# Kernel tuning notes

Measured on AMD Instinct MI355X. Metric: run time of the kernel, lower is better.

## Reference

```python
import jax, jax.numpy as jnp
import numpy as np

NUM_HEADS = 16
NUM_T = 8
L1D = 16  # img_size // patch_size


def _freqs_1d(dim, end, base=10000.0):
    f = 1.0 / (base ** (jnp.arange(0, dim, 2, dtype=jnp.float32) / dim))  # [dim/2]
    ang = jnp.outer(jnp.arange(end, dtype=jnp.float32), f)                # [end, dim/2]
    return jnp.cos(ang), jnp.sin(ang)


def _freqs_2d(dim, h, w, base=10000.0):
    f = 1.0 / (base ** (jnp.arange(0, dim, 4, dtype=jnp.float32)[: dim // 4] / dim))  # [dim/4]
    ax = jnp.outer(jnp.arange(w, dtype=jnp.float32), f)  # [w, dim/4]
    ay = jnp.outer(jnp.arange(h, dtype=jnp.float32), f)  # [h, dim/4]
    # flatten order: position index = y*w + x
    ang_x = jnp.broadcast_to(ax[None, :, :], (h, w, dim // 4)).reshape(h * w, dim // 4)
    ang_y = jnp.broadcast_to(ay[:, None, :], (h, w, dim // 4)).reshape(h * w, dim // 4)
    ang = jnp.concatenate([ang_x, ang_y], axis=-1)  # [h*w, dim/2]
    return jnp.cos(ang), jnp.sin(ang)


def _rope(x, cos, sin):
    # x: [..., P, d]; cos/sin: [P, d/2]; interleaved complex pairs (x0,x1),(x2,x3),...
    xr, xi = x[..., 0::2], x[..., 1::2]
    or_ = xr * cos - xi * sin
    oi = xr * sin + xi * cos
    return jnp.stack([or_, oi], axis=-1).reshape(x.shape)


def setup_inputs() -> dict:
    key = jax.random.key(0)
    ks = jax.random.split(key, 5)
    H = 1024
    return {
        "x": jax.random.normal(ks[0], (2, 2048, H), dtype=jnp.float32),
        "w_qkv": jax.random.normal(ks[1], (3 * H, H), dtype=jnp.float32) * 0.02,
        "b_qkv": jax.random.normal(ks[2], (3 * H,), dtype=jnp.float32) * 0.02,
        "w_out": jax.random.normal(ks[3], (H, H), dtype=jnp.float32) * 0.02,
        "b_out": jax.random.normal(ks[4], (H,), dtype=jnp.float32) * 0.02,
    }


def reference(x, w_qkv, b_qkv, w_out, b_out):
    B, L, H = x.shape
    n, t = NUM_HEADS, NUM_T
    hd = H // n
    Ls = L // t  # spatial tokens per frame (= L1D*L1D)

    # QKV projection; per-head layout [q|k|v] of size 3*hd (matches torch rearrange+chunk)
    qkv = (x @ w_qkv.T + b_qkv).reshape(B, L, n, 3 * hd)
    q, k, v = qkv[..., :hd], qkv[..., hd:2 * hd], qkv[..., 2 * hd:]

    cos_s, sin_s = _freqs_2d(hd, L1D, L1D)  # [Ls, hd/2]
    cos_t, sin_t = _freqs_1d(hd, t)         # [t, hd/2]

    def to_bntl(a):  # (B, L=t*Ls, n, hd) -> (B, n, t, Ls, hd)
        return a.reshape(B, t, Ls, n, hd).transpose(0, 3, 1, 2, 4)

    q = _rope(to_bntl(q), cos_s, sin_s)
    k = _rope(to_bntl(k), cos_s, sin_s)
    # temporal rope: rotate over t axis
    q = _rope(q.transpose(0, 1, 3, 2, 4), cos_t, sin_t).transpose(0, 1, 3, 2, 4)
    k = _rope(k.transpose(0, 1, 3, 2, 4), cos_t, sin_t).transpose(0, 1, 3, 2, 4)
    q = q.reshape(B, n, L, hd)
    k = k.reshape(B, n, L, hd)
    v = v.transpose(0, 2, 1, 3)  # (B, n, L, hd)

    scores = jnp.einsum('bnqd,bnkd->bnqk', q, k) / jnp.sqrt(jnp.asarray(hd, jnp.float32))
    idx = jnp.arange(L)
    neg = jnp.finfo(jnp.float32).min
    causal = jnp.where(idx[None, :] <= idx[:, None], 0.0, neg)  # [L, L]
    attn = jax.nn.softmax((scores + causal).astype(jnp.float32), axis=-1).astype(x.dtype)

    o = jnp.einsum('bnqk,bnkd->bnqd', attn, v).transpose(0, 2, 1, 3).reshape(B, L, H)
    o = o * jax.nn.sigmoid(o)  # swish
    return o @ w_out.T + b_out
```

## Files before the change

### kernel.cpp

```cpp
#include <hip/hip_runtime.h>
#include <math.h>

#define B_SZ 2
#define L_SEQ 2048
#define H_SZ 1024
#define NH 16
#define HD 64
#define QSCALE 0.18033688011112042f

typedef __attribute__((ext_vector_type(8))) short frag_ab;
typedef __attribute__((ext_vector_type(4))) float frag_cd;
typedef __attribute__((ext_vector_type(8))) unsigned short u16x8;
typedef __attribute__((ext_vector_type(4))) unsigned short u16x4;

__device__ __forceinline__ unsigned short f2bf(float f) {
  unsigned int x = __builtin_bit_cast(unsigned int, f);
  x += 0x7fffu + ((x >> 16) & 1u);
  return (unsigned short)(x >> 16);
}
__device__ __forceinline__ float bf2f(unsigned int u) {
  return __builtin_bit_cast(float, u << 16);
}
__device__ __forceinline__ unsigned int cvt_pk_bf16(float lo, float hi) {
  unsigned int r;
  asm("v_cvt_pk_bf16_f32 %0, %1, %2" : "=v"(r) : "v"(lo), "v"(hi));
  return r;
}
__device__ __forceinline__ void gload16(const void* g, void* l) {
  __builtin_amdgcn_global_load_lds((const __attribute__((address_space(1))) void*)g,
                                   (__attribute__((address_space(3))) void*)l, 16, 0, 0);
}

__device__ __forceinline__ void cvt8(const float* __restrict__ in,
                                     unsigned short* __restrict__ out, int i) {
  float4 a = *(const float4*)&in[i];
  float4 b = *(const float4*)&in[i + 4];
  u16x8 o = {f2bf(a.x), f2bf(a.y), f2bf(a.z), f2bf(a.w),
             f2bf(b.x), f2bf(b.y), f2bf(b.z), f2bf(b.w)};
  *(u16x8*)&out[i] = o;
}

#define SWZ32(row) ((((row) >> 1) & 3) << 3)

__global__ __launch_bounds__(256) void glue_pre_k(
    const float* __restrict__ x, const float* __restrict__ wq, const float* __restrict__ wo,
    unsigned short* __restrict__ xb, unsigned short* __restrict__ wqb,
    unsigned short* __restrict__ wob, float2* __restrict__ ctab) {
  int bx = blockIdx.x, tid = threadIdx.x;
  if (bx < 256) {
    int idx = bx * 256 + tid;
    int j = idx >> 11, l = idx & 2047;
    int ti = l >> 8;
    int s = l & 255;
    float ang_s;
    if (j < 16) ang_s = (float)(s & 15) * powf(10000.f, -(float)j / 16.f);
    else        ang_s = (float)(s >> 4) * powf(10000.f, -(float)(j - 16) / 16.f);
    float ang_t = (float)ti * powf(10000.f, -(float)j / 32.f);
    float a = ang_s + ang_t;
    ctab[idx] = make_float2(cosf(a), sinf(a));
  } else if (bx < 2304) {
    cvt8(x, xb, ((bx - 256) * 256 + tid) * 8);
  } else if (bx < 3840) {
    cvt8(wq, wqb, ((bx - 2304) * 256 + tid) * 8);
  } else {
    cvt8(wo, wob, ((bx - 3840) * 256 + tid) * 8);
  }
}

#define G_ISSUE(k0, bi)                                                        \
  _Pragma("unroll") for (int it = 0; it < 2; ++it) {                           \
    int c = tid + it * 256;                                                    \
    int row = c >> 2, e0 = ((c & 3) * 8) ^ SWZ32(row);                         \
    gload16(A + (size_t)(m0 + row) * K + (k0) + e0, &As[bi][c * 8]);           \
    gload16(W + (size_t)(n0 + row) * K + (k0) + e0, &Ws[bi][c * 8]);           \
  }

__global__ __launch_bounds__(256) void gemm_qkv_fused_k(
    const unsigned short* __restrict__ A, const unsigned short* __restrict__ W,
    const float* __restrict__ bias, const float2* __restrict__ ctab,
    unsigned short* __restrict__ Qb, unsigned short* __restrict__ Kb,
    unsigned short* __restrict__ Vt) {
  const int K = 1024, N = 3072;
  __shared__ unsigned short As[2][128 * 32];
  __shared__ unsigned short Ws[2][128 * 32];
  const frag_cd fzero = {0.f, 0.f, 0.f, 0.f};
  int tid = threadIdx.x;
  int nbx = N >> 7;
  int nwg = gridDim.x;
  int bid = blockIdx.x;
  int qq = nwg >> 3;
  int bidx = (bid & 7) * qq + (bid >> 3);
  int m0 = (bidx / nbx) * 128, n0 = (bidx % nbx) * 128;
  int w = tid >> 6, lane = tid & 63, t = lane & 15, g = lane >> 4;
  int wm = w >> 1, wn = w & 1;
  int fsw = (8 * g) ^ SWZ32(t);
  frag_cd acc[4][4];
#pragma unroll
  for (int mi = 0; mi < 4; ++mi)
#pragma unroll
    for (int ni = 0; ni < 4; ++ni) acc[mi][ni] = fzero;

  G_ISSUE(0, 0);
  __syncthreads();
  int kb = 0;
  for (int k0 = 0; k0 < K; k0 += 32, kb ^= 1) {
    if (k0 + 32 < K) { G_ISSUE(k0 + 32, kb ^ 1); }
    frag_ab af[4], wf[4];
#pragma unroll
    for (int mi = 0; mi < 4; ++mi)
      af[mi] = *(const frag_ab*)&As[kb][(wm * 64 + mi * 16 + t) * 32 + fsw];
#pragma unroll
    for (int ni = 0; ni < 4; ++ni)
      wf[ni] = *(const frag_ab*)&Ws[kb][(wn * 64 + ni * 16 + t) * 32 + fsw];
    __builtin_amdgcn_s_setprio(1);
#pragma unroll
    for (int mi = 0; mi < 4; ++mi)
#pragma unroll
      for (int ni = 0; ni < 4; ++ni)
        acc[mi][ni] = __builtin_amdgcn_mfma_f32_16x16x32_bf16(af[mi], wf[ni], acc[mi][ni], 0, 0, 0);
    __builtin_amdgcn_s_setprio(0);
    __syncthreads();
  }

#pragma unroll
  for (int ni = 0; ni < 4; ++ni) {
    int cb = n0 + wn * 64 + ni * 16;
    int region = (cb >> 6) % 3;
    int head = cb / 192;
    int d = (cb & 63) + t;
    float bv = bias[cb + t];
    if (region == 2) {
#pragma unroll
      for (int mi = 0; mi < 4; ++mi) {
        int row0 = m0 + wm * 64 + mi * 16 + g * 4;
        int bb = row0 >> 11, l0 = row0 & 2047;
        u16x4 ov;
#pragma unroll
        for (int r = 0; r < 4; ++r) ov[r] = f2bf(acc[mi][ni][r] + bv);
        *(u16x4*)&Vt[((size_t)((bb * NH + head) * HD + d)) * L_SEQ + l0] = ov;
      }
    } else {
      float qs = (region == 0) ? QSCALE : 1.f;
      float sgn = (t & 1) ? qs : -qs;
      unsigned short* dst = (region == 0) ? Qb : Kb;
      int j = d >> 1;
#pragma unroll
      for (int mi = 0; mi < 4; ++mi) {
        int row0 = m0 + wm * 64 + mi * 16 + g * 4;
        int bb = row0 >> 11, l0 = row0 & 2047;
        size_t obase = ((size_t)(bb * NH + head) * L_SEQ + l0) * HD + d;
        const float2* cp = ctab + (size_t)j * 2048 + l0;
        float4 v01 = *(const float4*)cp;
        float4 v23 = *(const float4*)(cp + 2);
        float cvec[4] = {v01.x, v01.z, v23.x, v23.z};
        float svec[4] = {v01.y, v01.w, v23.y, v23.w};
#pragma unroll
        for (int r = 0; r < 4; ++r) {
          float v = acc[mi][ni][r] + bv;
          float p = __shfl_xor(v, 1);
          float o = v * (cvec[r] * qs) + p * (svec[r] * sgn);
          dst[obase + (size_t)r * HD] = f2bf(o);
        }
      }
    }
  }
}

__global__ __launch_bounds__(256) void gemm_out_k(
    const unsigned short* __restrict__ A, const unsigned short* __restrict__ W,
    const float* __restrict__ bias, float* __restrict__ C, int M, int N, int K) {
  __shared__ unsigned short As[2][64 * 32];
  __shared__ unsigned short Ws[2][128 * 32];
  const frag_cd fzero = {0.f, 0.f, 0.f, 0.f};
  int tid = threadIdx.x;
  int nbx = N >> 7;
  int nwg = gridDim.x;
  int bid = blockIdx.x;
  int qq = nwg >> 3;
  int bidx = (bid & 7) * qq + (bid >> 3);
  int m0 = (bidx / nbx) * 64, n0 = (bidx % nbx) * 128;
  int w = tid >> 6, lane = tid & 63, t = lane & 15, g = lane >> 4;
  int wm = w >> 1, wn = w & 1;
  int fsw = (8 * g) ^ SWZ32(t);
  frag_cd acc[2][4];
#pragma unroll
  for (int mi = 0; mi < 2; ++mi)
#pragma unroll
    for (int ni = 0; ni < 4; ++ni) acc[mi][ni] = fzero;

#define G_ISSUE2(k0, bi)                                                       \
  {                                                                            \
    int rowA = tid >> 2, e0A = ((tid & 3) * 8) ^ SWZ32(rowA);                  \
    gload16(A + (size_t)(m0 + rowA) * K + (k0) + e0A, &As[bi][tid * 8]);       \
    _Pragma("unroll") for (int it = 0; it < 2; ++it) {                         \
      int c = tid + it * 256;                                                  \
      int row = c >> 2, e0 = ((c & 3) * 8) ^ SWZ32(row);                       \
      gload16(W + (size_t)(n0 + row) * K + (k0) + e0, &Ws[bi][c * 8]);         \
    }                                                                          \
  }

  G_ISSUE2(0, 0);
  __syncthreads();
  int kb = 0;
  for (int k0 = 0; k0 < K; k0 += 32, kb ^= 1) {
    if (k0 + 32 < K) { G_ISSUE2(k0 + 32, kb ^ 1); }
    frag_ab af[2], wf[4];
#pragma unroll
    for (int mi = 0; mi < 2; ++mi)
      af[mi] = *(const frag_ab*)&As[kb][(wm * 32 + mi * 16 + t) * 32 + fsw];
#pragma unroll
    for (int ni = 0; ni < 4; ++ni)
      wf[ni] = *(const frag_ab*)&Ws[kb][(wn * 64 + ni * 16 + t) * 32 + fsw];
    __builtin_amdgcn_s_setprio(1);
#pragma unroll
    for (int mi = 0; mi < 2; ++mi)
#pragma unroll
      for (int ni = 0; ni < 4; ++ni)
        acc[mi][ni] = __builtin_amdgcn_mfma_f32_16x16x32_bf16(af[mi], wf[ni], acc[mi][ni], 0, 0, 0);
    __builtin_amdgcn_s_setprio(0);
    __syncthreads();
  }
#pragma unroll
  for (int mi = 0; mi < 2; ++mi)
#pragma unroll
    for (int ni = 0; ni < 4; ++ni) {
      int col = n0 + wn * 64 + ni * 16 + t;
      float bv = bias[col];
#pragma unroll
      for (int r = 0; r < 4; ++r)
        C[(size_t)(m0 + wm * 32 + mi * 16 + g * 4 + r) * N + col] = acc[mi][ni][r] + bv;
    }
}

__device__ __forceinline__ void attn_tile(
    const unsigned short* __restrict__ Ksb, const unsigned short* __restrict__ Vsb,
    unsigned short* __restrict__ pw,
    const frag_ab* qf, frag_cd* oacc, float& l_run,
    int qrow, bool diag, int kt, int t, int g) {
  const frag_cd cinit = {-32.f, -32.f, -32.f, -32.f};
  frag_cd st[4];
  __builtin_amdgcn_s_setprio(1);
#pragma unroll
  for (int kb = 0; kb < 4; ++kb) {
    frag_ab k0f = *(const frag_ab*)&Ksb[(((kb * 16 + t) * 64) + 8 * g) ^ ((t & 7) << 3)];
    frag_ab k1f = *(const frag_ab*)&Ksb[(((kb * 16 + t) * 64) + 32 + 8 * g) ^ ((t & 7) << 3)];
    st[kb] = __builtin_amdgcn_mfma_f32_16x16x32_bf16(k0f, qf[0], cinit, 0, 0, 0);
    st[kb] = __builtin_amdgcn_mfma_f32_16x16x32_bf16(k1f, qf[1], st[kb], 0, 0, 0);
  }
  __builtin_amdgcn_s_setprio(0);
  float psum = 0.f;
  unsigned int pk[8];
#pragma unroll
  for (int i = 0; i < 8; ++i) {
    int kb = i >> 1, r0 = (2 * i) & 3;
    float x0 = st[kb][r0], x1 = st[kb][r0 + 1];
    if (diag) {
      if ((kt * 64 + kb * 16 + g * 4 + r0) > qrow) x0 = -1e30f;
      if ((kt * 64 + kb * 16 + g * 4 + r0 + 1) > qrow) x1 = -1e30f;
    }
    float p0 = __builtin_amdgcn_exp2f(x0);
    float p1 = __builtin_amdgcn_exp2f(x1);
    psum += p0 + p1;
    pk[i] = cvt_pk_bf16(p0, p1);
  }
  psum += __shfl_xor(psum, 16);
  psum += __shfl_xor(psum, 32);
  l_run += psum;

#pragma unroll
  for (int kb = 0; kb < 4; ++kb) {
    uint2 pr = {pk[kb * 2], pk[kb * 2 + 1]};
    *(uint2*)&pw[(t * 64 + kb * 16 + g * 4) ^ ((t & 7) << 3)] = pr;
  }
  frag_ab pf0 = *(const frag_ab*)&pw[(t * 64 + 8 * g) ^ ((t & 7) << 3)];
  frag_ab pf1 = *(const frag_ab*)&pw[(t * 64 + 32 + 8 * g) ^ ((t & 7) << 3)];
  __builtin_amdgcn_s_setprio(1);
#pragma unroll
  for (int db = 0; db < 4; ++db) {
    frag_ab v0f = *(const frag_ab*)&Vsb[(((db * 16 + t) * 64) + 8 * g) ^ ((t & 7) << 3)];
    frag_ab v1f = *(const frag_ab*)&Vsb[(((db * 16 + t) * 64) + 32 + 8 * g) ^ ((t & 7) << 3)];
    oacc[db] = __builtin_amdgcn_mfma_f32_16x16x32_bf16(v0f, pf0, oacc[db], 0, 0, 0);
    oacc[db] = __builtin_amdgcn_mfma_f32_16x16x32_bf16(v1f, pf1, oacc[db], 0, 0, 0);
  }
  __builtin_amdgcn_s_setprio(0);
}

__global__ __launch_bounds__(512) void attn_mfma_k(
    const unsigned short* __restrict__ Qg, const unsigned short* __restrict__ Kg,
    const unsigned short* __restrict__ Vt, unsigned short* __restrict__ Og) {
  __shared__ unsigned short Ks[2][64 * 64];
  __shared__ unsigned short Vs[2][64 * 64];
  __shared__ unsigned short Ps[8][16 * 64];
  const frag_cd fzero = {0.f, 0.f, 0.f, 0.f};
  int bx = blockIdx.x;
  int qtA = bx & 15;
  int n = (bx >> 4) & 15;
  int b = bx >> 8;
  int qtB = 31 - qtA;
  int tid = threadIdx.x;
  int w = tid >> 6, lane = tid & 63, t = lane & 15, g = lane >> 4;
  int side = w >> 2;
  int qt = side ? qtA : qtB;
  size_t kvbase = ((size_t)(b * NH + n)) * L_SEQ * HD;
  int qrow = qt * 64 + (w & 3) * 16 + t;

  const unsigned short* qp = Qg + kvbase + (size_t)qrow * HD;
  frag_ab qf[2] = {*(const frag_ab*)(qp + 8 * g), *(const frag_ab*)(qp + 32 + 8 * g)};

  frag_cd oacc[4];
#pragma unroll
  for (int db = 0; db < 4; ++db) oacc[db] = fzero;
  float l_run = 0.f;

  int srow = tid >> 3, se0 = (tid & 7) * 8;
  int sdst = (srow * 64 + se0) ^ ((srow & 7) << 3);
  u16x8 kreg = *(const u16x8*)(Kg + kvbase + (size_t)srow * HD + se0);
  u16x8 vreg = *(const u16x8*)(Vt + kvbase + (size_t)srow * L_SEQ + se0);
  *(u16x8*)&Ks[0][sdst] = kreg;
  *(u16x8*)&Vs[0][sdst] = vreg;

  for (int kt = 0; kt <= qtB; ++kt) {
    int cur = kt & 1;
    __syncthreads();
    if (kt < qtB) {
      kreg = *(const u16x8*)(Kg + kvbase + (size_t)((kt + 1) * 64 + srow) * HD + se0);
      vreg = *(const u16x8*)(Vt + kvbase + (size_t)srow * L_SEQ + (kt + 1) * 64 + se0);
    }
    if (kt <= qt)
      attn_tile(&Ks[cur][0], &Vs[cur][0], &Ps[w][0], qf, oacc, l_run, qrow,
                kt == qt, kt, t, g);
    if (kt < qtB) {
      int nxt = cur ^ 1;
      *(u16x8*)&Ks[nxt][sdst] = kreg;
      *(u16x8*)&Vs[nxt][sdst] = vreg;
    }
  }

  size_t ob0 = (size_t)b * L_SEQ * H_SZ + n * 64;
  float inv = 1.f / l_run;
#pragma unroll
  for (int db = 0; db < 4; ++db) {
    u16x4 ov;
#pragma unroll
    for (int r = 0; r < 4; ++r) {
      float o = oacc[db][r] * inv;
      o = o / (1.f + __expf(-o));
      ov[r] = f2bf(o);
    }
    *(u16x4*)&Og[ob0 + (size_t)qrow * H_SZ + db * 16 + g * 4] = ov;
  }
}

extern "C" void kernel_launch(void* const* d_in, const int* in_sizes, int n_in,
                              void* d_out, int out_size, void* d_ws, size_t ws_size,
                              hipStream_t stream) {
  const float* x = (const float*)d_in[0];
  const float* w_qkv = (const float*)d_in[1];
  const float* b_qkv = (const float*)d_in[2];
  const float* w_out = (const float*)d_in[3];
  const float* b_out = (const float*)d_in[4];
  float* out = (float*)d_out;

  float* ws = (float*)d_ws;
  float2* ctab = (float2*)ws;
  unsigned short* us = (unsigned short*)(ws + 131072);
  unsigned short* Qb = us;
  unsigned short* Kb = Qb + 4194304;
  unsigned short* Vt = Kb + 4194304;
  unsigned short* Og = Vt + 4194304;
  unsigned short* xb = Og + 4194304;
  unsigned short* wqkvb = xb + 4194304;
  unsigned short* woutb = wqkvb + 3145728;

  glue_pre_k<<<4352, 256, 0, stream>>>(x, w_qkv, w_out, xb, wqkvb, woutb, ctab);

  gemm_qkv_fused_k<<<768, 256, 0, stream>>>(xb, wqkvb, b_qkv, ctab, Qb, Kb, Vt);

  attn_mfma_k<<<B_SZ * NH * 16, 512, 0, stream>>>(Qb, Kb, Vt, Og);

  gemm_out_k<<<512, 256, 0, stream>>>(Og, woutb, b_out, out, 4096, 1024, 1024);
}
```

Measured before the change: 107.7 us.

## Process both paired query tiles per wave to reuse K/V fragments

The attention kernel drops from 512 to 256 threads per block. Each wave now handles one 16-row slice of both the long and the short query tile, so K and V fragments read from shared memory once serve both tiles. The row-sum shuffle reduction moves out of the loop to the epilogue, and the global prefetch is issued two tiles ahead. The cost is more registers per thread from two accumulator sets, fewer waves per block, and a serial dependence between the two tiles inside one wave.

```diff
diff --git a/kernel.cpp b/kernel.cpp
--- a/kernel.cpp
+++ b/kernel.cpp
@@ -232,66 +232,15 @@
     }
 }
 
-__device__ __forceinline__ void attn_tile(
-    const unsigned short* __restrict__ Ksb, const unsigned short* __restrict__ Vsb,
-    unsigned short* __restrict__ pw,
-    const frag_ab* qf, frag_cd* oacc, float& l_run,
-    int qrow, bool diag, int kt, int t, int g) {
-  const frag_cd cinit = {-32.f, -32.f, -32.f, -32.f};
-  frag_cd st[4];
-  __builtin_amdgcn_s_setprio(1);
-#pragma unroll
-  for (int kb = 0; kb < 4; ++kb) {
-    frag_ab k0f = *(const frag_ab*)&Ksb[(((kb * 16 + t) * 64) + 8 * g) ^ ((t & 7) << 3)];
-    frag_ab k1f = *(const frag_ab*)&Ksb[(((kb * 16 + t) * 64) + 32 + 8 * g) ^ ((t & 7) << 3)];
-    st[kb] = __builtin_amdgcn_mfma_f32_16x16x32_bf16(k0f, qf[0], cinit, 0, 0, 0);
-    st[kb] = __builtin_amdgcn_mfma_f32_16x16x32_bf16(k1f, qf[1], st[kb], 0, 0, 0);
-  }
-  __builtin_amdgcn_s_setprio(0);
-  float psum = 0.f;
-  unsigned int pk[8];
-#pragma unroll
-  for (int i = 0; i < 8; ++i) {
-    int kb = i >> 1, r0 = (2 * i) & 3;
-    float x0 = st[kb][r0], x1 = st[kb][r0 + 1];
-    if (diag) {
-      if ((kt * 64 + kb * 16 + g * 4 + r0) > qrow) x0 = -1e30f;
-      if ((kt * 64 + kb * 16 + g * 4 + r0 + 1) > qrow) x1 = -1e30f;
-    }
-    float p0 = __builtin_amdgcn_exp2f(x0);
-    float p1 = __builtin_amdgcn_exp2f(x1);
-    psum += p0 + p1;
-    pk[i] = cvt_pk_bf16(p0, p1);
-  }
-  psum += __shfl_xor(psum, 16);
-  psum += __shfl_xor(psum, 32);
-  l_run += psum;
-
-#pragma unroll
-  for (int kb = 0; kb < 4; ++kb) {
-    uint2 pr = {pk[kb * 2], pk[kb * 2 + 1]};
-    *(uint2*)&pw[(t * 64 + kb * 16 + g * 4) ^ ((t & 7) << 3)] = pr;
-  }
-  frag_ab pf0 = *(const frag_ab*)&pw[(t * 64 + 8 * g) ^ ((t & 7) << 3)];
-  frag_ab pf1 = *(const frag_ab*)&pw[(t * 64 + 32 + 8 * g) ^ ((t & 7) << 3)];
-  __builtin_amdgcn_s_setprio(1);
-#pragma unroll
-  for (int db = 0; db < 4; ++db) {
-    frag_ab v0f = *(const frag_ab*)&Vsb[(((db * 16 + t) * 64) + 8 * g) ^ ((t & 7) << 3)];
-    frag_ab v1f = *(const frag_ab*)&Vsb[(((db * 16 + t) * 64) + 32 + 8 * g) ^ ((t & 7) << 3)];
-    oacc[db] = __builtin_amdgcn_mfma_f32_16x16x32_bf16(v0f, pf0, oacc[db], 0, 0, 0);
-    oacc[db] = __builtin_amdgcn_mfma_f32_16x16x32_bf16(v1f, pf1, oacc[db], 0, 0, 0);
-  }
-  __builtin_amdgcn_s_setprio(0);
-}
-
-__global__ __launch_bounds__(512) void attn_mfma_k(
+__global__ __launch_bounds__(256) void attn_mfma_k(
     const unsigned short* __restrict__ Qg, const unsigned short* __restrict__ Kg,
     const unsigned short* __restrict__ Vt, unsigned short* __restrict__ Og) {
   __shared__ unsigned short Ks[2][64 * 64];
   __shared__ unsigned short Vs[2][64 * 64];
-  __shared__ unsigned short Ps[8][16 * 64];
+  __shared__ unsigned short PsL[4][16 * 64];
+  __shared__ unsigned short PsS[4][16 * 64];
   const frag_cd fzero = {0.f, 0.f, 0.f, 0.f};
+  const frag_cd cinit = {-32.f, -32.f, -32.f, -32.f};
   int bx = blockIdx.x;
   int qtA = bx & 15;
   int n = (bx >> 4) & 15;
@@ -299,55 +248,175 @@
   int qtB = 31 - qtA;
   int tid = threadIdx.x;
   int w = tid >> 6, lane = tid & 63, t = lane & 15, g = lane >> 4;
-  int side = w >> 2;
-  int qt = side ? qtA : qtB;
   size_t kvbase = ((size_t)(b * NH + n)) * L_SEQ * HD;
-  int qrow = qt * 64 + (w & 3) * 16 + t;
-
-  const unsigned short* qp = Qg + kvbase + (size_t)qrow * HD;
-  frag_ab qf[2] = {*(const frag_ab*)(qp + 8 * g), *(const frag_ab*)(qp + 32 + 8 * g)};
-
-  frag_cd oacc[4];
-#pragma unroll
-  for (int db = 0; db < 4; ++db) oacc[db] = fzero;
-  float l_run = 0.f;
+  int qrowL = qtB * 64 + w * 16 + t;
+  int qrowS = qtA * 64 + w * 16 + t;
+  unsigned short* pwL = &PsL[w][0];
+  unsigned short* pwS = &PsS[w][0];
+
+  const unsigned short* qpL = Qg + kvbase + (size_t)qrowL * HD;
+  const unsigned short* qpS = Qg + kvbase + (size_t)qrowS * HD;
+  frag_ab qfL0 = *(const frag_ab*)(qpL + 8 * g), qfL1 = *(const frag_ab*)(qpL + 32 + 8 * g);
+  frag_ab qfS0 = *(const frag_ab*)(qpS + 8 * g), qfS1 = *(const frag_ab*)(qpS + 32 + 8 * g);
+
+  frag_cd oaccL[4], oaccS[4];
+#pragma unroll
+  for (int db = 0; db < 4; ++db) { oaccL[db] = fzero; oaccS[db] = fzero; }
+  float lLp = 0.f, lSp = 0.f;
 
   int srow = tid >> 3, se0 = (tid & 7) * 8;
-  int sdst = (srow * 64 + se0) ^ ((srow & 7) << 3);
-  u16x8 kreg = *(const u16x8*)(Kg + kvbase + (size_t)srow * HD + se0);
-  u16x8 vreg = *(const u16x8*)(Vt + kvbase + (size_t)srow * L_SEQ + se0);
-  *(u16x8*)&Ks[0][sdst] = kreg;
-  *(u16x8*)&Vs[0][sdst] = vreg;
+  int sd0 = (srow * 64 + se0) ^ ((srow & 7) << 3);
+  int sd1 = ((srow + 32) * 64 + se0) ^ ((srow & 7) << 3);
+  u16x8 kreg0 = *(const u16x8*)(Kg + kvbase + (size_t)srow * HD + se0);
+  u16x8 kreg1 = *(const u16x8*)(Kg + kvbase + (size_t)(srow + 32) * HD + se0);
+  u16x8 vreg0 = *(const u16x8*)(Vt + kvbase + (size_t)srow * L_SEQ + se0);
+  u16x8 vreg1 = *(const u16x8*)(Vt + kvbase + (size_t)(srow + 32) * L_SEQ + se0);
+  *(u16x8*)&Ks[0][sd0] = kreg0;
+  *(u16x8*)&Ks[0][sd1] = kreg1;
+  *(u16x8*)&Vs[0][sd0] = vreg0;
+  *(u16x8*)&Vs[0][sd1] = vreg1;
+  if (qtB > 0) {
+    kreg0 = *(const u16x8*)(Kg + kvbase + (size_t)(64 + srow) * HD + se0);
+    kreg1 = *(const u16x8*)(Kg + kvbase + (size_t)(96 + srow) * HD + se0);
+    vreg0 = *(const u16x8*)(Vt + kvbase + (size_t)srow * L_SEQ + 64 + se0);
+    vreg1 = *(const u16x8*)(Vt + kvbase + (size_t)(srow + 32) * L_SEQ + 64 + se0);
+  }
 
   for (int kt = 0; kt <= qtB; ++kt) {
-    int cur = kt & 1;
+    int cur = kt & 1, nxt = cur ^ 1;
     __syncthreads();
     if (kt < qtB) {
-      kreg = *(const u16x8*)(Kg + kvbase + (size_t)((kt + 1) * 64 + srow) * HD + se0);
-      vreg = *(const u16x8*)(Vt + kvbase + (size_t)srow * L_SEQ + (kt + 1) * 64 + se0);
-    }
-    if (kt <= qt)
-      attn_tile(&Ks[cur][0], &Vs[cur][0], &Ps[w][0], qf, oacc, l_run, qrow,
-                kt == qt, kt, t, g);
-    if (kt < qtB) {
-      int nxt = cur ^ 1;
-      *(u16x8*)&Ks[nxt][sdst] = kreg;
-      *(u16x8*)&Vs[nxt][sdst] = vreg;
+      *(u16x8*)&Ks[nxt][sd0] = kreg0;
+      *(u16x8*)&Ks[nxt][sd1] = kreg1;
+      *(u16x8*)&Vs[nxt][sd0] = vreg0;
+      *(u16x8*)&Vs[nxt][sd1] = vreg1;
+    }
+    if (kt + 1 < qtB) {
+      kreg0 = *(const u16x8*)(Kg + kvbase + (size_t)((kt + 2) * 64 + srow) * HD + se0);
+      kreg1 = *(const u16x8*)(Kg + kvbase + (size_t)((kt + 2) * 64 + 32 + srow) * HD + se0);
+      vreg0 = *(const u16x8*)(Vt + kvbase + (size_t)srow * L_SEQ + (kt + 2) * 64 + se0);
+      vreg1 = *(const u16x8*)(Vt + kvbase + (size_t)(srow + 32) * L_SEQ + (kt + 2) * 64 + se0);
+    }
+    bool doS = (kt <= qtA);
+
+    frag_ab k0f[4], k1f[4];
+#pragma unroll
+    for (int kb = 0; kb < 4; ++kb) {
+      k0f[kb] = *(const frag_ab*)&Ks[cur][(((kb * 16 + t) * 64) + 8 * g) ^ ((t & 7) << 3)];
+      k1f[kb] = *(const frag_ab*)&Ks[cur][(((kb * 16 + t) * 64) + 32 + 8 * g) ^ ((t & 7) << 3)];
+    }
+    frag_cd stL[4], stS[4];
+    __builtin_amdgcn_s_setprio(1);
+#pragma unroll
+    for (int kb = 0; kb < 4; ++kb) {
+      stL[kb] = __builtin_amdgcn_mfma_f32_16x16x32_bf16(k0f[kb], qfL0, cinit, 0, 0, 0);
+      stL[kb] = __builtin_amdgcn_mfma_f32_16x16x32_bf16(k1f[kb], qfL1, stL[kb], 0, 0, 0);
+    }
+    if (doS) {
+#pragma unroll
+      for (int kb = 0; kb < 4; ++kb) {
+        stS[kb] = __builtin_amdgcn_mfma_f32_16x16x32_bf16(k0f[kb], qfS0, cinit, 0, 0, 0);
+        stS[kb] = __builtin_amdgcn_mfma_f32_16x16x32_bf16(k1f[kb], qfS1, stS[kb], 0, 0, 0);
+      }
+    }
+    __builtin_amdgcn_s_setprio(0);
+
+    frag_ab v0f[4], v1f[4];
+#pragma unroll
+    for (int db = 0; db < 4; ++db) {
+      v0f[db] = *(const frag_ab*)&Vs[cur][(((db * 16 + t) * 64) + 8 * g) ^ ((t & 7) << 3)];
+      v1f[db] = *(const frag_ab*)&Vs[cur][(((db * 16 + t) * 64) + 32 + 8 * g) ^ ((t & 7) << 3)];
+    }
+
+    {
+      bool diag = (kt == qtB);
+      unsigned int pk[8];
+#pragma unroll
+      for (int i = 0; i < 8; ++i) {
+        int kb = i >> 1, r0 = (2 * i) & 3;
+        float x0 = stL[kb][r0], x1 = stL[kb][r0 + 1];
+        if (diag) {
+          if ((kt * 64 + kb * 16 + g * 4 + r0) > qrowL) x0 = -1e30f;
+          if ((kt * 64 + kb * 16 + g * 4 + r0 + 1) > qrowL) x1 = -1e30f;
+        }
+        float p0 = __builtin_amdgcn_exp2f(x0);
+        float p1 = __builtin_amdgcn_exp2f(x1);
+        lLp += p0 + p1;
+        pk[i] = cvt_pk_bf16(p0, p1);
+      }
+#pragma unroll
+      for (int kb = 0; kb < 4; ++kb) {
+        uint2 pr = {pk[kb * 2], pk[kb * 2 + 1]};
+        *(uint2*)&pwL[(t * 64 + kb * 16 + g * 4) ^ ((t & 7) << 3)] = pr;
+      }
+    }
+    if (doS) {
+      bool diag = (kt == qtA);
+      unsigned int pk[8];
+#pragma unroll
+      for (int i = 0; i < 8; ++i) {
+        int kb = i >> 1, r0 = (2 * i) & 3;
+        float x0 = stS[kb][r0], x1 = stS[kb][r0 + 1];
+        if (diag) {
+          if ((kt * 64 + kb * 16 + g * 4 + r0) > qrowS) x0 = -1e30f;
+          if ((kt * 64 + kb * 16 + g * 4 + r0 + 1) > qrowS) x1 = -1e30f;
+        }
+        float p0 = __builtin_amdgcn_exp2f(x0);
+        float p1 = __builtin_amdgcn_exp2f(x1);
+        lSp += p0 + p1;
+        pk[i] = cvt_pk_bf16(p0, p1);
+      }
+#pragma unroll
+      for (int kb = 0; kb < 4; ++kb) {
+        uint2 pr = {pk[kb * 2], pk[kb * 2 + 1]};
+        *(uint2*)&pwS[(t * 64 + kb * 16 + g * 4) ^ ((t & 7) << 3)] = pr;
+      }
+    }
+
+    {
+      frag_ab pf0 = *(const frag_ab*)&pwL[(t * 64 + 8 * g) ^ ((t & 7) << 3)];
+      frag_ab pf1 = *(const frag_ab*)&pwL[(t * 64 + 32 + 8 * g) ^ ((t & 7) << 3)];
+      __builtin_amdgcn_s_setprio(1);
+#pragma unroll
+      for (int db = 0; db < 4; ++db) {
+        oaccL[db] = __builtin_amdgcn_mfma_f32_16x16x32_bf16(v0f[db], pf0, oaccL[db], 0, 0, 0);
+        oaccL[db] = __builtin_amdgcn_mfma_f32_16x16x32_bf16(v1f[db], pf1, oaccL[db], 0, 0, 0);
+      }
+      __builtin_amdgcn_s_setprio(0);
+    }
+    if (doS) {
+      frag_ab pf0 = *(const frag_ab*)&pwS[(t * 64 + 8 * g) ^ ((t & 7) << 3)];
+      frag_ab pf1 = *(const frag_ab*)&pwS[(t * 64 + 32 + 8 * g) ^ ((t & 7) << 3)];
+      __builtin_amdgcn_s_setprio(1);
+#pragma unroll
+      for (int db = 0; db < 4; ++db) {
+        oaccS[db] = __builtin_amdgcn_mfma_f32_16x16x32_bf16(v0f[db], pf0, oaccS[db], 0, 0, 0);
+        oaccS[db] = __builtin_amdgcn_mfma_f32_16x16x32_bf16(v1f[db], pf1, oaccS[db], 0, 0, 0);
+      }
+      __builtin_amdgcn_s_setprio(0);
     }
   }
 
   size_t ob0 = (size_t)b * L_SEQ * H_SZ + n * 64;
-  float inv = 1.f / l_run;
-#pragma unroll
-  for (int db = 0; db < 4; ++db) {
-    u16x4 ov;
-#pragma unroll
-    for (int r = 0; r < 4; ++r) {
-      float o = oacc[db][r] * inv;
-      o = o / (1.f + __expf(-o));
-      ov[r] = f2bf(o);
-    }
-    *(u16x4*)&Og[ob0 + (size_t)qrow * H_SZ + db * 16 + g * 4] = ov;
+#pragma unroll
+  for (int side = 0; side < 2; ++side) {
+    float lp = side ? lSp : lLp;
+    float l_run = lp + __shfl_xor(lp, 16);
+    l_run += __shfl_xor(l_run, 32);
+    float inv = 1.f / l_run;
+    frag_cd* oacc = side ? oaccS : oaccL;
+    int qrow = side ? qrowS : qrowL;
+#pragma unroll
+    for (int db = 0; db < 4; ++db) {
+      u16x4 ov;
+#pragma unroll
+      for (int r = 0; r < 4; ++r) {
+        float o = oacc[db][r] * inv;
+        o = o / (1.f + __expf(-o));
+        ov[r] = f2bf(o);
+      }
+      *(u16x4*)&Og[ob0 + (size_t)qrow * H_SZ + db * 16 + g * 4] = ov;
+    }
   }
 }
 
@@ -376,7 +445,7 @@
 
   gemm_qkv_fused_k<<<768, 256, 0, stream>>>(xb, wqkvb, b_qkv, ctab, Qb, Kb, Vt);
 
-  attn_mfma_k<<<B_SZ * NH * 16, 512, 0, stream>>>(Qb, Kb, Vt, Og);
+  attn_mfma_k<<<B_SZ * NH * 16, 256, 0, stream>>>(Qb, Kb, Vt, Og);
 
   gemm_out_k<<<512, 256, 0, stream>>>(Og, woutb, b_out, out, 4096, 1024, 1024);
 }
```

After: 106.3 us (median of 3 runs). About the same (-1.3%).
